# Kernel tuning notes

Hardware: AMD Instinct MI355X
Metric: run time of the kernel (lower is better)

The kernel has to match this reference:

```python
import jax, jax.numpy as jnp
import numpy as np

B, V, D, H = 128, 32, 64, 256
E = V * (V - 1)  # 992 directed edges (no self loops)
_edges = np.ones((V, V)) - np.eye(V)
SEND, RECV = np.where(_edges)  # each len E


def _mlp(x, w1, b1, w2, b2, w3, b3):
    h = jax.nn.relu(x @ w1.T + b1)
    h = jax.nn.relu(h @ w2.T + b2)
    return h @ w3.T + b3


def setup_inputs() -> dict:
    key = jax.random.key(0)
    ks = iter(jax.random.split(key, 48))
    def w(shape, scale=0.05):
        return jax.random.normal(next(ks), shape, jnp.float32) * scale
    d = {}
    d['inputs'] = jax.random.normal(next(ks), (B, V, D), jnp.float32)
    d['h0'] = jax.random.normal(next(ks), (B, E, H), jnp.float32) * 0.1
    d['c0'] = jax.random.normal(next(ks), (B, E, H), jnp.float32) * 0.1
    for name, ind in (('m1', D), ('m2', 2 * H), ('m3', H), ('m4', 3 * H)):
        d[name + 'w1'] = w((H, ind)); d[name + 'b1'] = jnp.full((H,), 0.1, jnp.float32)
        d[name + 'w2'] = w((H, H));   d[name + 'b2'] = jnp.full((H,), 0.1, jnp.float32)
        d[name + 'w3'] = w((H, H));   d[name + 'b3'] = jnp.full((H,), 0.1, jnp.float32)
    d['wih'] = w((4 * H, H)); d['whh'] = w((4 * H, H))
    d['bih'] = jnp.zeros((4 * H,), jnp.float32); d['bhh'] = jnp.zeros((4 * H,), jnp.float32)
    d['pw1'] = w((H, H)); d['pb1'] = jnp.full((H,), 0.1, jnp.float32)
    d['pw2'] = w((H, H)); d['pb2'] = jnp.full((H,), 0.1, jnp.float32)
    d['pw3'] = w((2, H)); d['pb3'] = jnp.full((2,), 0.1, jnp.float32)
    return d


def reference(inputs, h0, c0,
              m1w1, m1b1, m1w2, m1b2, m1w3, m1b3,
              m2w1, m2b1, m2w2, m2b2, m2w3, m2b3,
              m3w1, m3b1, m3w2, m3b2, m3w3, m3b3,
              m4w1, m4b1, m4w2, m4b2, m4w3, m4b3,
              wih, whh, bih, bhh,
              pw1, pb1, pw2, pb2, pw3, pb3):
    send, recv = jnp.asarray(SEND), jnp.asarray(RECV)
    # edge2node one-hot matrix [V, E] (fixed, non-trainable in original)
    e2n = (recv[None, :] == jnp.arange(V)[:, None]).astype(inputs.dtype)

    x = _mlp(inputs, m1w1, m1b1, m1w2, m1b2, m1w3, m1b3)          # [B,V,H]
    x = jnp.concatenate([x[:, send], x[:, recv]], axis=-1)         # [B,E,2H]
    x = _mlp(x, m2w1, m2b1, m2w2, m2b2, m2w3, m2b3)                # [B,E,H]
    x_skip = x
    x = jnp.einsum('ve,beh->bvh', e2n, x) / (V - 1)                # [B,V,H]
    x = _mlp(x, m3w1, m3b1, m3w2, m3b2, m3w3, m3b3)                # [B,V,H]
    x = jnp.concatenate([x[:, send], x[:, recv], x_skip], axis=-1)  # [B,E,3H]
    x = _mlp(x, m4w1, m4b1, m4w2, m4b2, m4w3, m4b3)                # [B,E,H]

    # single-step LSTM over B*E independent sequences of length 1
    gates = x @ wih.T + bih + h0 @ whh.T + bhh                     # [B,E,4H]
    i, f, g, o = jnp.split(gates, 4, axis=-1)
    c1 = jax.nn.sigmoid(f) * c0 + jax.nn.sigmoid(i) * jnp.tanh(g)
    h1 = jax.nn.sigmoid(o) * jnp.tanh(c1)

    prior_result = _mlp(h1, pw1, pb1, pw2, pb2, pw3, pb3)          # [B,E,2]
    return prior_result, h1, c1
```

## Files before the change

### kernel.cpp

```cpp
#include <hip/hip_runtime.h>
#include <math.h>

#define B_ 128
#define V_ 32
#define D_ 64
#define H_ 256
#define E_ 992
#define ME (B_*E_)
#define MV (B_*V_)

typedef __attribute__((ext_vector_type(8))) short bf8v;
typedef __attribute__((ext_vector_type(4))) float f4v;
typedef __attribute__((ext_vector_type(8))) unsigned short u16x8;

__device__ __forceinline__ unsigned short f2bf(float f) {
    union { float f; unsigned int u; } v; v.f = f;
    unsigned int u = v.u + 0x7FFFu + ((v.u >> 16) & 1u);
    return (unsigned short)(u >> 16);
}
__device__ __forceinline__ float bf2f(unsigned short h) {
    union { unsigned int u; float f; } v; v.u = ((unsigned int)h) << 16;
    return v.f;
}
__device__ __forceinline__ float sigf(float x) {
    x = fminf(fmaxf(x, -30.f), 30.f);
    return 1.f / (1.f + __expf(-x));
}
__device__ __forceinline__ float tanhf_fast(float x) {
    x = fminf(fmaxf(x, -15.f), 15.f);
    float e = __expf(2.f * x);
    return (e - 1.f) / (e + 1.f);
}
__device__ __forceinline__ void gl_lds16(const unsigned short* g, unsigned short* l) {
    __builtin_amdgcn_global_load_lds(
        (const __attribute__((address_space(1))) unsigned int*)g,
        (__attribute__((address_space(3))) unsigned int*)l, 16, 0, 0);
}

__device__ __forceinline__ int tidx(int row, int k) {
    return row * 256 + (k ^ ((row & 7) << 3));
}

__global__ __launch_bounds__(256)
void f2b_k(const float* __restrict__ s, unsigned short* __restrict__ d, int n4)
{
    const int g = blockIdx.x * 256 + threadIdx.x;
    if (g >= n4) return;
    const float4 v = ((const float4*)s)[g];
    ushort4 o;
    o.x = f2bf(v.x); o.y = f2bf(v.y); o.z = f2bf(v.z); o.w = f2bf(v.w);
    ((ushort4*)d)[g] = o;
}

__global__ __launch_bounds__(256)
void f2bs_k(const float* __restrict__ s, unsigned short* __restrict__ d,
            int rows, int cols4, int ld, int off)
{
    const int g = blockIdx.x * 256 + threadIdx.x;
    if (g >= rows * cols4) return;
    const int r = g / cols4, c4 = g - r * cols4;
    const float4 v = *(const float4*)(s + (size_t)r * ld + off + c4 * 4);
    ushort4 o;
    o.x = f2bf(v.x); o.y = f2bf(v.y); o.z = f2bf(v.z); o.w = f2bf(v.w);
    *(ushort4*)(d + (size_t)r * cols4 * 4 + c4 * 4) = o;
}

__global__ __launch_bounds__(256)
void gemm_k(const float* __restrict__ A, int lda,
            const float* __restrict__ W, int ldw,
            const float* __restrict__ bias,
            float* __restrict__ out,
            int M, int N, int K, int do_relu)
{
    __shared__ float As[32][68];
    __shared__ float Ws[32][68];
    const int m0 = blockIdx.x * 64;
    const int n0 = blockIdx.y * 64;
    const int t  = threadIdx.x;
    const int tx = t & 15, ty = t >> 4;
    const int lm = t >> 3;
    const int lk = (t & 7) * 4;

    float acc[4][4] = {};

    for (int k0 = 0; k0 < K; k0 += 32) {
        #pragma unroll
        for (int h = 0; h < 2; ++h) {
            const int m = m0 + lm + h * 32;
            const float4 v = *(const float4*)(A + (size_t)m * lda + k0 + lk);
            As[lk + 0][lm + h * 32] = v.x;
            As[lk + 1][lm + h * 32] = v.y;
            As[lk + 2][lm + h * 32] = v.z;
            As[lk + 3][lm + h * 32] = v.w;
            const int n = n0 + lm + h * 32;
            const float4 w = *(const float4*)(W + (size_t)n * ldw + k0 + lk);
            Ws[lk + 0][lm + h * 32] = w.x;
            Ws[lk + 1][lm + h * 32] = w.y;
            Ws[lk + 2][lm + h * 32] = w.z;
            Ws[lk + 3][lm + h * 32] = w.w;
        }
        __syncthreads();
        #pragma unroll
        for (int kk = 0; kk < 32; ++kk) {
            float a[4], b[4];
            #pragma unroll
            for (int i = 0; i < 4; ++i) a[i] = As[kk][ty * 4 + i];
            #pragma unroll
            for (int j = 0; j < 4; ++j) b[j] = Ws[kk][tx * 4 + j];
            #pragma unroll
            for (int i = 0; i < 4; ++i)
                #pragma unroll
                for (int j = 0; j < 4; ++j)
                    acc[i][j] = fmaf(a[i], b[j], acc[i][j]);
        }
        __syncthreads();
    }

    #pragma unroll
    for (int i = 0; i < 4; ++i) {
        const int m = m0 + ty * 4 + i;
        const size_t ob = (size_t)m * N;
        #pragma unroll
        for (int j = 0; j < 4; ++j) {
            const int n = n0 + tx * 4 + j;
            float v = acc[i][j];
            if (bias) v += bias[n];
            if (do_relu) v = fmaxf(v, 0.f);
            out[ob + n] = v;
        }
    }
}

template<int RELU, int EPI>
__device__ __forceinline__ void chain_gemm(
    unsigned short* T, unsigned short* Wst,
    const unsigned short* __restrict__ W, const float* __restrict__ bias,
    int m0, const float* __restrict__ ES, const float* __restrict__ ER)
{
    const int t = threadIdx.x, lane = t & 63, wid = t >> 6;
    const int r = wid >> 2, c = wid & 3;
    const int kof = (lane >> 4) * 8;
    const int ra = r * 64 + (lane & 15);
    const int q1 = t & 255, kp1 = t >> 8;

    f4v acc[4][4];
    #pragma unroll
    for (int i = 0; i < 4; ++i)
        #pragma unroll
        for (int j = 0; j < 4; ++j)
            acc[i][j] = (f4v){0.f, 0.f, 0.f, 0.f};

    gl_lds16(W + (size_t)q1 * 256 + kp1 * 8,       Wst + t * 8);
    gl_lds16(W + (size_t)q1 * 256 + (kp1 + 2) * 8, Wst + 4096 + t * 8);
    __syncthreads();
    int cur = 0;
    #pragma unroll
    for (int s = 0; s < 8; ++s) {
        if (s < 7) {
            const int k0 = (s + 1) * 32;
            gl_lds16(W + (size_t)q1 * 256 + k0 + kp1 * 8,       Wst + (cur ^ 1) * 8192 + t * 8);
            gl_lds16(W + (size_t)q1 * 256 + k0 + (kp1 + 2) * 8, Wst + (cur ^ 1) * 8192 + 4096 + t * 8);
        }
        bf8v a[4], b[4];
        #pragma unroll
        for (int f = 0; f < 4; ++f) {
            const int rr = ra + f * 16;
            a[f] = *(const bf8v*)&T[tidx(rr, s * 32 + kof)];
            b[f] = *(const bf8v*)&Wst[cur * 8192 + (lane >> 4) * 2048 + (c * 64 + f * 16 + (lane & 15)) * 8];
        }
        #pragma unroll
        for (int i = 0; i < 4; ++i)
            #pragma unroll
            for (int j = 0; j < 4; ++j)
                acc[i][j] = __builtin_amdgcn_mfma_f32_16x16x32_bf16(a[i], b[j], acc[i][j], 0, 0, 0);
        __syncthreads();
        cur ^= 1;
    }

    float bv[4];
    #pragma unroll
    for (int nf = 0; nf < 4; ++nf) bv[nf] = bias[c * 64 + nf * 16 + (lane & 15)];

    #pragma unroll
    for (int mf = 0; mf < 4; ++mf) {
        #pragma unroll
        for (int reg = 0; reg < 4; ++reg) {
            const int row = r * 64 + mf * 16 + (lane >> 4) * 4 + reg;
            size_t bs = 0, br = 0;
            if (EPI) {
                const int m  = m0 + row;
                const int bb = m / E_;
                const int e  = m - bb * E_;
                const int sS = e / 31;
                const int jj = e - sS * 31;
                const int rr = jj + (jj >= sS ? 1 : 0);
                bs = ((size_t)bb * V_ + sS) * H_;
                br = ((size_t)bb * V_ + rr) * H_;
            }
            #pragma unroll
            for (int nf = 0; nf < 4; ++nf) {
                const int n = c * 64 + nf * 16 + (lane & 15);
                float v = acc[mf][nf][reg] + bv[nf];
                if (EPI) v += ES[bs + n] + ER[br + n];
                if (RELU) v = fmaxf(v, 0.f);
                T[tidx(row, n)] = f2bf(v);
            }
        }
    }
    __syncthreads();
}

__global__ __launch_bounds__(512, 2)
void chain1_k(const float* __restrict__ Ys, const float* __restrict__ Yr,
              const float* __restrict__ b1,
              const unsigned short* __restrict__ w2, const float* __restrict__ b2,
              const unsigned short* __restrict__ w3, const float* __restrict__ b3,
              unsigned short* __restrict__ X2out)
{
    __shared__ alignas(16) unsigned short T[32768];
    __shared__ alignas(16) unsigned short Wst[16384];
    const int t  = threadIdx.x;
    const int m0 = blockIdx.x * 128;

    #pragma unroll
    for (int it = 0; it < 16; ++it) {
        const int q   = it * 512 + t;
        const int row = q >> 6;
        const int n4  = (q & 63) * 4;
        const int m  = m0 + row;
        const int bb = m / E_;
        const int e  = m - bb * E_;
        const int s  = e / 31;
        const int jj = e - s * 31;
        const int rv = jj + (jj >= s ? 1 : 0);
        const float4 ys = *(const float4*)&Ys[((size_t)bb * V_ + s)  * H_ + n4];
        const float4 yr = *(const float4*)&Yr[((size_t)bb * V_ + rv) * H_ + n4];
        const float4 bx = *(const float4*)&b1[n4];
        ushort4 o;
        o.x = f2bf(fmaxf(ys.x + yr.x + bx.x, 0.f));
        o.y = f2bf(fmaxf(ys.y + yr.y + bx.y, 0.f));
        o.z = f2bf(fmaxf(ys.z + yr.z + bx.z, 0.f));
        o.w = f2bf(fmaxf(ys.w + yr.w + bx.w, 0.f));
        *(ushort4*)&T[tidx(row, n4)] = o;
    }
    __syncthreads();

    chain_gemm<1, 0>(T, Wst, w2, b2, m0, nullptr, nullptr);
    chain_gemm<0, 0>(T, Wst, w3, b3, m0, nullptr, nullptr);

    #pragma unroll
    for (int it = 0; it < 8; ++it) {
        const int g   = it * 512 + t;
        const int row = g >> 5;
        const int kp  = (g & 31) * 8;
        *(u16x8*)&X2out[(size_t)(m0 + row) * 256 + kp] = *(const u16x8*)&T[tidx(row, kp)];
    }
}

__device__ __forceinline__ void lstm_pass(
    const unsigned short* T, unsigned short* Wst, unsigned short* Ast,
    const unsigned short* __restrict__ h0b,
    const unsigned short* __restrict__ wih, const unsigned short* __restrict__ whh,
    const float* __restrict__ bih, const float* __restrict__ bhh,
    const float* __restrict__ c0,
    float* __restrict__ h1, float* __restrict__ c1, unsigned short* __restrict__ h1b,
    int m0, int jc)
{
    const int t = threadIdx.x, lane = t & 63, wid = t >> 6;
    const int r = wid >> 2, c = wid & 3;
    const int kof = (lane >> 4) * 8;
    const int ra = r * 64 + (lane & 15);
    const int q1 = t & 255, kp1 = t >> 8;
    const size_t grow = (size_t)((q1 >> 6) * 256 + jc * 64 + (q1 & 63)) * 256;
    const int qa = t & 127, kpa = t >> 7;

    f4v acc[4][4];
    #pragma unroll
    for (int i = 0; i < 4; ++i)
        #pragma unroll
        for (int j = 0; j < 4; ++j)
            acc[i][j] = (f4v){0.f, 0.f, 0.f, 0.f};

    gl_lds16(wih + grow + kp1 * 8,       Wst + t * 8);
    gl_lds16(wih + grow + (kp1 + 2) * 8, Wst + 4096 + t * 8);
    __syncthreads();
    int cur = 0;
    #pragma unroll
    for (int s = 0; s < 16; ++s) {
        if (s < 15) {
            const int s2 = s + 1;
            const unsigned short* Wm = (s2 < 8) ? wih : whh;
            const int k0 = (s2 & 7) * 32;
            gl_lds16(Wm + grow + k0 + kp1 * 8,       Wst + (cur ^ 1) * 8192 + t * 8);
            gl_lds16(Wm + grow + k0 + (kp1 + 2) * 8, Wst + (cur ^ 1) * 8192 + 4096 + t * 8);
            if (s2 >= 8) {
                const int ka = (s2 - 8) * 32;
                gl_lds16(h0b + (size_t)(m0 + qa) * 256 + ka + kpa * 8, Ast + (cur ^ 1) * 4096 + t * 8);
            }
        }
        bf8v a[4], b[4];
        #pragma unroll
        for (int f = 0; f < 4; ++f) {
            const int rr = ra + f * 16;
            if (s < 8) a[f] = *(const bf8v*)&T[tidx(rr, s * 32 + kof)];
            else       a[f] = *(const bf8v*)&Ast[cur * 4096 + (lane >> 4) * 1024 + rr * 8];
            b[f] = *(const bf8v*)&Wst[cur * 8192 + (lane >> 4) * 2048 + (f * 64 + c * 16 + (lane & 15)) * 8];
        }
        #pragma unroll
        for (int i = 0; i < 4; ++i)
            #pragma unroll
            for (int g = 0; g < 4; ++g)
                acc[i][g] = __builtin_amdgcn_mfma_f32_16x16x32_bf16(a[i], b[g], acc[i][g], 0, 0, 0);
        __syncthreads();
        cur ^= 1;
    }

    const int j = jc * 64 + c * 16 + (lane & 15);
    const float bi0 = bih[j]       + bhh[j];
    const float bi1 = bih[256 + j] + bhh[256 + j];
    const float bi2 = bih[512 + j] + bhh[512 + j];
    const float bi3 = bih[768 + j] + bhh[768 + j];
    #pragma unroll
    for (int mf = 0; mf < 4; ++mf) {
        #pragma unroll
        for (int reg = 0; reg < 4; ++reg) {
            const int row = r * 64 + mf * 16 + (lane >> 4) * 4 + reg;
            const size_t o = (size_t)(m0 + row) * 256 + j;
            const float gi = acc[mf][0][reg] + bi0;
            const float gf = acc[mf][1][reg] + bi1;
            const float gg = acc[mf][2][reg] + bi2;
            const float go = acc[mf][3][reg] + bi3;
            const float cn = sigf(gf) * c0[o] + sigf(gi) * tanhf_fast(gg);
            const float hn = sigf(go) * tanhf_fast(cn);
            c1[o] = cn;
            h1[o] = hn;
            h1b[o] = f2bf(hn);
        }
    }
    __syncthreads();
}

__global__ __launch_bounds__(512, 2)
void chain2_k(const unsigned short* __restrict__ X2,
              const unsigned short* __restrict__ w41, const float* __restrict__ b41,
              const unsigned short* __restrict__ w42, const float* __restrict__ b42,
              const unsigned short* __restrict__ w43, const float* __restrict__ b43,
              const float* __restrict__ ZS, const float* __restrict__ ZR,
              const unsigned short* __restrict__ h0b,
              const unsigned short* __restrict__ wih, const unsigned short* __restrict__ whh,
              const float* __restrict__ bih, const float* __restrict__ bhh,
              const float* __restrict__ c0,
              float* __restrict__ h1, float* __restrict__ c1,
              unsigned short* __restrict__ h1b)
{
    __shared__ alignas(16) unsigned short T[32768];
    __shared__ alignas(16) unsigned short Wst[16384];
    __shared__ alignas(16) unsigned short Ast[8192];
    const int t  = threadIdx.x;
    const int m0 = blockIdx.x * 128;

    #pragma unroll
    for (int it = 0; it < 8; ++it) {
        const int g   = it * 512 + t;
        const int row = g >> 5;
        const int kp  = (g & 31) * 8;
        *(u16x8*)&T[tidx(row, kp)] = *(const u16x8*)&X2[(size_t)(m0 + row) * 256 + kp];
    }
    __syncthreads();

    chain_gemm<1, 1>(T, Wst, w41, b41, m0, ZS, ZR);
    chain_gemm<1, 0>(T, Wst, w42, b42, m0, nullptr, nullptr);
    chain_gemm<0, 0>(T, Wst, w43, b43, m0, nullptr, nullptr);

    for (int jc = 0; jc < 4; ++jc)
        lstm_pass(T, Wst, Ast, h0b, wih, whh, bih, bhh, c0, h1, c1, h1b, m0, jc);
}

__global__ __launch_bounds__(512, 2)
void prior_k(const unsigned short* __restrict__ Hin,
             const unsigned short* __restrict__ w1, const float* __restrict__ b1,
             const unsigned short* __restrict__ w2, const float* __restrict__ b2,
             const float* __restrict__ w3, const float* __restrict__ b3,
             float* __restrict__ out)
{
    __shared__ alignas(16) unsigned short T[32768];
    __shared__ alignas(16) unsigned short Wst[16384];
    const int t  = threadIdx.x;
    const int m0 = blockIdx.x * 128;

    #pragma unroll
    for (int it = 0; it < 8; ++it) {
        const int g   = it * 512 + t;
        const int row = g >> 5;
        const int kp  = (g & 31) * 8;
        *(u16x8*)&T[tidx(row, kp)] = *(const u16x8*)&Hin[(size_t)(m0 + row) * 256 + kp];
    }
    __syncthreads();

    chain_gemm<1, 0>(T, Wst, w1, b1, m0, nullptr, nullptr);
    chain_gemm<1, 0>(T, Wst, w2, b2, m0, nullptr, nullptr);

    const int row = t >> 2;
    const int kb  = (t & 3) * 64;
    float p0 = 0.f, p1 = 0.f;
    #pragma unroll
    for (int g = 0; g < 8; ++g) {
        const int k = kb + g * 8;
        const u16x8 v = *(const u16x8*)&T[tidx(row, k)];
        #pragma unroll
        for (int i = 0; i < 8; ++i) {
            const float x = bf2f(v[i]);
            p0 += x * w3[k + i];
            p1 += x * w3[256 + k + i];
        }
    }
    p0 += __shfl_xor(p0, 1); p0 += __shfl_xor(p0, 2);
    p1 += __shfl_xor(p1, 1); p1 += __shfl_xor(p1, 2);
    if ((t & 3) == 0) {
        out[(size_t)(m0 + row) * 2 + 0] = p0 + b3[0];
        out[(size_t)(m0 + row) * 2 + 1] = p1 + b3[1];
    }
}

__global__ __launch_bounds__(256)
void agg_k(const unsigned short* __restrict__ X2, float* __restrict__ outv)
{
    const int g = blockIdx.x * 256 + threadIdx.x;
    const int h = g & 255;
    const int v = (g >> 8) & 31;
    const int b = g >> 13;
    float s = 0.f;
    #pragma unroll
    for (int snd = 0; snd < 32; ++snd) {
        if (snd == v) continue;
        const int e = snd * 31 + v - (snd < v ? 1 : 0);
        s += bf2f(X2[((size_t)b * E_ + e) * H_ + h]);
    }
    outv[g] = s * (1.f / 31.f);
}

extern "C" void kernel_launch(void* const* d_in, const int* in_sizes, int n_in,
                              void* d_out, int out_size, void* d_ws, size_t ws_size,
                              hipStream_t stream)
{
    const float* inputs = (const float*)d_in[0];
    const float* h0     = (const float*)d_in[1];
    const float* c0     = (const float*)d_in[2];
    const float* m1w1 = (const float*)d_in[3];  const float* m1b1 = (const float*)d_in[4];
    const float* m1w2 = (const float*)d_in[5];  const float* m1b2 = (const float*)d_in[6];
    const float* m1w3 = (const float*)d_in[7];  const float* m1b3 = (const float*)d_in[8];
    const float* m2w1 = (const float*)d_in[9];  const float* m2b1 = (const float*)d_in[10];
    const float* m2w2 = (const float*)d_in[11]; const float* m2b2 = (const float*)d_in[12];
    const float* m2w3 = (const float*)d_in[13]; const float* m2b3 = (const float*)d_in[14];
    const float* m3w1 = (const float*)d_in[15]; const float* m3b1 = (const float*)d_in[16];
    const float* m3w2 = (const float*)d_in[17]; const float* m3b2 = (const float*)d_in[18];
    const float* m3w3 = (const float*)d_in[19]; const float* m3b3 = (const float*)d_in[20];
    const float* m4w1 = (const float*)d_in[21]; const float* m4b1 = (const float*)d_in[22];
    const float* m4w2 = (const float*)d_in[23]; const float* m4b2 = (const float*)d_in[24];
    const float* m4w3 = (const float*)d_in[25]; const float* m4b3 = (const float*)d_in[26];
    const float* wih  = (const float*)d_in[27]; const float* whh  = (const float*)d_in[28];
    const float* bih  = (const float*)d_in[29]; const float* bhh  = (const float*)d_in[30];
    const float* pw1  = (const float*)d_in[31]; const float* pb1  = (const float*)d_in[32];
    const float* pw2  = (const float*)d_in[33]; const float* pb2  = (const float*)d_in[34];
    const float* pw3  = (const float*)d_in[35]; const float* pb3  = (const float*)d_in[36];

    float* out   = (float*)d_out;
    float* prior = out;
    float* h1    = out + (size_t)ME * 2;
    float* c1    = h1 + (size_t)ME * H_;

    float* S0 = (float*)d_ws;
    float* S1 = S0 + (size_t)MV * H_;
    float* S2 = S1 + (size_t)MV * H_;
    float* S3 = S2 + (size_t)MV * H_;
    unsigned short* EA = (unsigned short*)(S3 + (size_t)MV * H_);
    unsigned short* EB = EA + (size_t)ME * H_;
    unsigned short* EC = EB + (size_t)ME * H_;
    unsigned short* cw22 = EC + (size_t)ME * H_;
    unsigned short* cw23 = cw22 + 65536;
    unsigned short* cw41 = cw23 + 65536;
    unsigned short* cw42 = cw41 + 65536;
    unsigned short* cw43 = cw42 + 65536;
    unsigned short* cpw1 = cw43 + 65536;
    unsigned short* cpw2 = cpw1 + 65536;
    unsigned short* cwih = cpw2 + 65536;
    unsigned short* cwhh = cwih + 262144;

    const dim3 blk(256);
    const dim3 blk5(512);
    const dim3 gV(MV / 64, 4);
    const dim3 gC(ME / 128);

    f2b_k<<<64, blk, 0, stream>>>(m2w2, cw22, 16384);
    f2b_k<<<64, blk, 0, stream>>>(m2w3, cw23, 16384);
    f2bs_k<<<64, blk, 0, stream>>>(m4w1, cw41, 256, 64, 768, 512);
    f2b_k<<<64, blk, 0, stream>>>(m4w2, cw42, 16384);
    f2b_k<<<64, blk, 0, stream>>>(m4w3, cw43, 16384);
    f2b_k<<<64, blk, 0, stream>>>(pw1, cpw1, 16384);
    f2b_k<<<64, blk, 0, stream>>>(pw2, cpw2, 16384);
    f2b_k<<<256, blk, 0, stream>>>(wih, cwih, 65536);
    f2b_k<<<256, blk, 0, stream>>>(whh, cwhh, 65536);
    f2b_k<<<ME * H_ / 1024, blk, 0, stream>>>(h0, EB, ME * H_ / 4);

    gemm_k<<<gV, blk, 0, stream>>>(inputs, 64, m1w1, 64, m1b1, S0, MV, 256, 64, 1);
    gemm_k<<<gV, blk, 0, stream>>>(S0, 256, m1w2, 256, m1b2, S1, MV, 256, 256, 1);
    gemm_k<<<gV, blk, 0, stream>>>(S1, 256, m1w3, 256, m1b3, S0, MV, 256, 256, 0);

    gemm_k<<<gV, blk, 0, stream>>>(S0, 256, m2w1,       512, nullptr, S2, MV, 256, 256, 0);
    gemm_k<<<gV, blk, 0, stream>>>(S0, 256, m2w1 + 256, 512, nullptr, S3, MV, 256, 256, 0);

    chain1_k<<<gC, blk5, 0, stream>>>(S2, S3, m2b1, cw22, m2b2, cw23, m2b3, EA);

    agg_k<<<MV * H_ / 256, blk, 0, stream>>>(EA, S0);
    gemm_k<<<gV, blk, 0, stream>>>(S0, 256, m3w1, 256, m3b1, S1, MV, 256, 256, 1);
    gemm_k<<<gV, blk, 0, stream>>>(S1, 256, m3w2, 256, m3b2, S0, MV, 256, 256, 1);
    gemm_k<<<gV, blk, 0, stream>>>(S0, 256, m3w3, 256, m3b3, S1, MV, 256, 256, 0);

    gemm_k<<<gV, blk, 0, stream>>>(S1, 256, m4w1,       768, nullptr, S2, MV, 256, 256, 0);
    gemm_k<<<gV, blk, 0, stream>>>(S1, 256, m4w1 + 256, 768, nullptr, S3, MV, 256, 256, 0);

    chain2_k<<<gC, blk5, 0, stream>>>(EA, cw41, m4b1, cw42, m4b2, cw43, m4b3,
                                      S2, S3, EB, cwih, cwhh, bih, bhh, c0, h1, c1, EC);

    prior_k<<<gC, blk5, 0, stream>>>(EC, cpw1, pb1, cpw2, pb2, pw3, pb3, prior);
}
```

Before: 1.382 ms.

## Load MFMA weight fragments directly from global into registers, halve chain tiles

The fused chain kernels (edge MLPs, LSTM, prior MLP) no longer stage weights through LDS with global_load_lds double buffering. Each wave now reads its B fragments straight from global memory (L2-resident bf16 weights) into registers, prefetching one k-step ahead, and the LSTM h0 operand is read the same way. The row tile drops from 128 to 64 with 256-thread blocks, which cuts LDS use and removes the per-k-step barriers, so more blocks can be resident per CU. The nine weight conversion launches are merged into two batched kernels. In exchange, weight fetches are repeated per wave from global/L2 instead of shared through LDS, and global-load latency now sits closer to the MFMA loop.

Result: slower. 3.935 ms (+184.8%).

```diff
diff --git a/kernel.cpp b/kernel.cpp
--- a/kernel.cpp
+++ b/kernel.cpp
@@ -31,14 +31,43 @@
     float e = __expf(2.f * x);
     return (e - 1.f) / (e + 1.f);
 }
-__device__ __forceinline__ void gl_lds16(const unsigned short* g, unsigned short* l) {
-    __builtin_amdgcn_global_load_lds(
-        (const __attribute__((address_space(1))) unsigned int*)g,
-        (__attribute__((address_space(3))) unsigned int*)l, 16, 0, 0);
-}
 
 __device__ __forceinline__ int tidx(int row, int k) {
     return row * 256 + (k ^ ((row & 7) << 3));
+}
+
+__global__ __launch_bounds__(256)
+void convW7_k(const float* __restrict__ s0, const float* __restrict__ s1,
+              const float* __restrict__ s2, const float* __restrict__ s3,
+              const float* __restrict__ s4, const float* __restrict__ s5,
+              const float* __restrict__ s6, unsigned short* __restrict__ d)
+{
+    const int y = blockIdx.y;
+    const int g = blockIdx.x * 256 + threadIdx.x;
+    float4 v;
+    if (y == 2) {
+        const int r = g >> 6, c4 = (g & 63) * 4;
+        v = *(const float4*)(s2 + (size_t)r * 768 + 512 + c4);
+    } else {
+        const float* s = (y == 0) ? s0 : (y == 1) ? s1 : (y == 3) ? s3 :
+                         (y == 4) ? s4 : (y == 5) ? s5 : s6;
+        v = ((const float4*)s)[g];
+    }
+    ushort4 o;
+    o.x = f2bf(v.x); o.y = f2bf(v.y); o.z = f2bf(v.z); o.w = f2bf(v.w);
+    ((ushort4*)(d + (size_t)y * 65536))[g] = o;
+}
+
+__global__ __launch_bounds__(256)
+void convIH_k(const float* __restrict__ wih, const float* __restrict__ whh,
+              unsigned short* __restrict__ d)
+{
+    const int y = blockIdx.y;
+    const int g = blockIdx.x * 256 + threadIdx.x;
+    const float4 v = ((const float4*)(y ? whh : wih))[g];
+    ushort4 o;
+    o.x = f2bf(v.x); o.y = f2bf(v.y); o.z = f2bf(v.z); o.w = f2bf(v.w);
+    ((ushort4*)(d + (size_t)y * 262144))[g] = o;
 }
 
 __global__ __launch_bounds__(256)
@@ -50,19 +79,6 @@
     ushort4 o;
     o.x = f2bf(v.x); o.y = f2bf(v.y); o.z = f2bf(v.z); o.w = f2bf(v.w);
     ((ushort4*)d)[g] = o;
-}
-
-__global__ __launch_bounds__(256)
-void f2bs_k(const float* __restrict__ s, unsigned short* __restrict__ d,
-            int rows, int cols4, int ld, int off)
-{
-    const int g = blockIdx.x * 256 + threadIdx.x;
-    if (g >= rows * cols4) return;
-    const int r = g / cols4, c4 = g - r * cols4;
-    const float4 v = *(const float4*)(s + (size_t)r * ld + off + c4 * 4);
-    ushort4 o;
-    o.x = f2bf(v.x); o.y = f2bf(v.y); o.z = f2bf(v.z); o.w = f2bf(v.w);
-    *(ushort4*)(d + (size_t)r * cols4 * 4 + c4 * 4) = o;
 }
 
 __global__ __launch_bounds__(256)
@@ -132,16 +148,14 @@
 }
 
 template<int RELU, int EPI>
-__device__ __forceinline__ void chain_gemm(
-    unsigned short* T, unsigned short* Wst,
+__device__ __forceinline__ void chain_layer(
+    unsigned short* T,
     const unsigned short* __restrict__ W, const float* __restrict__ bias,
     int m0, const float* __restrict__ ES, const float* __restrict__ ER)
 {
-    const int t = threadIdx.x, lane = t & 63, wid = t >> 6;
-    const int r = wid >> 2, c = wid & 3;
-    const int kof = (lane >> 4) * 8;
-    const int ra = r * 64 + (lane & 15);
-    const int q1 = t & 255, kp1 = t >> 8;
+    const int t = threadIdx.x, lane = t & 63, c = t >> 6;
+    const int laneN = lane & 15, kof = (lane >> 4) * 8;
+    const unsigned short* wb = W + (size_t)(c * 64 + laneN) * 256 + kof;
 
     f4v acc[4][4];
     #pragma unroll
@@ -150,42 +164,40 @@
         for (int j = 0; j < 4; ++j)
             acc[i][j] = (f4v){0.f, 0.f, 0.f, 0.f};
 
-    gl_lds16(W + (size_t)q1 * 256 + kp1 * 8,       Wst + t * 8);
-    gl_lds16(W + (size_t)q1 * 256 + (kp1 + 2) * 8, Wst + 4096 + t * 8);
+    bf8v bc[4];
+    #pragma unroll
+    for (int f = 0; f < 4; ++f) bc[f] = *(const bf8v*)(wb + f * 4096);
+
+    #pragma unroll
+    for (int s = 0; s < 8; ++s) {
+        bf8v bn[4];
+        if (s < 7) {
+            #pragma unroll
+            for (int f = 0; f < 4; ++f) bn[f] = *(const bf8v*)(wb + f * 4096 + (s + 1) * 32);
+        }
+        bf8v a[4];
+        #pragma unroll
+        for (int i = 0; i < 4; ++i) a[i] = *(const bf8v*)&T[tidx(i * 16 + laneN, s * 32 + kof)];
+        #pragma unroll
+        for (int i = 0; i < 4; ++i)
+            #pragma unroll
+            for (int j = 0; j < 4; ++j)
+                acc[i][j] = __builtin_amdgcn_mfma_f32_16x16x32_bf16(a[i], bc[j], acc[i][j], 0, 0, 0);
+        #pragma unroll
+        for (int f = 0; f < 4; ++f) bc[f] = bn[f];
+    }
+
     __syncthreads();
-    int cur = 0;
-    #pragma unroll
-    for (int s = 0; s < 8; ++s) {
-        if (s < 7) {
-            const int k0 = (s + 1) * 32;
-            gl_lds16(W + (size_t)q1 * 256 + k0 + kp1 * 8,       Wst + (cur ^ 1) * 8192 + t * 8);
-            gl_lds16(W + (size_t)q1 * 256 + k0 + (kp1 + 2) * 8, Wst + (cur ^ 1) * 8192 + 4096 + t * 8);
-        }
-        bf8v a[4], b[4];
-        #pragma unroll
-        for (int f = 0; f < 4; ++f) {
-            const int rr = ra + f * 16;
-            a[f] = *(const bf8v*)&T[tidx(rr, s * 32 + kof)];
-            b[f] = *(const bf8v*)&Wst[cur * 8192 + (lane >> 4) * 2048 + (c * 64 + f * 16 + (lane & 15)) * 8];
-        }
-        #pragma unroll
-        for (int i = 0; i < 4; ++i)
-            #pragma unroll
-            for (int j = 0; j < 4; ++j)
-                acc[i][j] = __builtin_amdgcn_mfma_f32_16x16x32_bf16(a[i], b[j], acc[i][j], 0, 0, 0);
-        __syncthreads();
-        cur ^= 1;
-    }
 
     float bv[4];
     #pragma unroll
-    for (int nf = 0; nf < 4; ++nf) bv[nf] = bias[c * 64 + nf * 16 + (lane & 15)];
-
-    #pragma unroll
-    for (int mf = 0; mf < 4; ++mf) {
+    for (int j = 0; j < 4; ++j) bv[j] = bias[c * 64 + j * 16 + laneN];
+
+    #pragma unroll
+    for (int i = 0; i < 4; ++i) {
         #pragma unroll
         for (int reg = 0; reg < 4; ++reg) {
-            const int row = r * 64 + mf * 16 + (lane >> 4) * 4 + reg;
+            const int row = i * 16 + (lane >> 4) * 4 + reg;
             size_t bs = 0, br = 0;
             if (EPI) {
                 const int m  = m0 + row;
@@ -198,9 +210,9 @@
                 br = ((size_t)bb * V_ + rr) * H_;
             }
             #pragma unroll
-            for (int nf = 0; nf < 4; ++nf) {
-                const int n = c * 64 + nf * 16 + (lane & 15);
-                float v = acc[mf][nf][reg] + bv[nf];
+            for (int j = 0; j < 4; ++j) {
+                const int n = c * 64 + j * 16 + laneN;
+                float v = acc[i][j][reg] + bv[j];
                 if (EPI) v += ES[bs + n] + ER[br + n];
                 if (RELU) v = fmaxf(v, 0.f);
                 T[tidx(row, n)] = f2bf(v);
@@ -210,21 +222,95 @@
     __syncthreads();
 }
 
-__global__ __launch_bounds__(512, 2)
+__device__ __forceinline__ void lstm_pass(
+    const unsigned short* T,
+    const unsigned short* __restrict__ h0b,
+    const unsigned short* __restrict__ wih, const unsigned short* __restrict__ whh,
+    const float* __restrict__ bih, const float* __restrict__ bhh,
+    const float* __restrict__ c0,
+    float* __restrict__ h1, float* __restrict__ c1, unsigned short* __restrict__ h1b,
+    int m0, int jc)
+{
+    const int t = threadIdx.x, lane = t & 63, c = t >> 6;
+    const int laneN = lane & 15, kof = (lane >> 4) * 8;
+    const unsigned short* wbi = wih + (size_t)(jc * 64 + c * 16 + laneN) * 256 + kof;
+    const unsigned short* wbh = whh + (size_t)(jc * 64 + c * 16 + laneN) * 256 + kof;
+    const unsigned short* ab  = h0b + (size_t)(m0 + laneN) * 256 + kof;
+
+    f4v acc[4][4];
+    #pragma unroll
+    for (int i = 0; i < 4; ++i)
+        #pragma unroll
+        for (int g = 0; g < 4; ++g)
+            acc[i][g] = (f4v){0.f, 0.f, 0.f, 0.f};
+
+    bf8v bc[4];
+    #pragma unroll
+    for (int g = 0; g < 4; ++g) bc[g] = *(const bf8v*)(wbi + (size_t)g * 65536);
+
+    #pragma unroll
+    for (int s = 0; s < 16; ++s) {
+        bf8v bn[4];
+        if (s < 15) {
+            const int s2 = s + 1;
+            #pragma unroll
+            for (int g = 0; g < 4; ++g)
+                bn[g] = (s2 < 8) ? *(const bf8v*)(wbi + (size_t)g * 65536 + s2 * 32)
+                                 : *(const bf8v*)(wbh + (size_t)g * 65536 + (s2 - 8) * 32);
+        }
+        bf8v a[4];
+        #pragma unroll
+        for (int i = 0; i < 4; ++i) {
+            if (s < 8) a[i] = *(const bf8v*)&T[tidx(i * 16 + laneN, s * 32 + kof)];
+            else       a[i] = *(const bf8v*)(ab + (size_t)i * 4096 + (s - 8) * 32);
+        }
+        #pragma unroll
+        for (int i = 0; i < 4; ++i)
+            #pragma unroll
+            for (int g = 0; g < 4; ++g)
+                acc[i][g] = __builtin_amdgcn_mfma_f32_16x16x32_bf16(a[i], bc[g], acc[i][g], 0, 0, 0);
+        #pragma unroll
+        for (int g = 0; g < 4; ++g) bc[g] = bn[g];
+    }
+
+    const int j = jc * 64 + c * 16 + laneN;
+    const float bi0 = bih[j]       + bhh[j];
+    const float bi1 = bih[256 + j] + bhh[256 + j];
+    const float bi2 = bih[512 + j] + bhh[512 + j];
+    const float bi3 = bih[768 + j] + bhh[768 + j];
+    #pragma unroll
+    for (int i = 0; i < 4; ++i) {
+        #pragma unroll
+        for (int reg = 0; reg < 4; ++reg) {
+            const int row = i * 16 + (lane >> 4) * 4 + reg;
+            const size_t o = (size_t)(m0 + row) * 256 + j;
+            const float gi = acc[i][0][reg] + bi0;
+            const float gf = acc[i][1][reg] + bi1;
+            const float gg = acc[i][2][reg] + bi2;
+            const float go = acc[i][3][reg] + bi3;
+            const float cn = sigf(gf) * c0[o] + sigf(gi) * tanhf_fast(gg);
+            const float hn = sigf(go) * tanhf_fast(cn);
+            c1[o] = cn;
+            h1[o] = hn;
+            h1b[o] = f2bf(hn);
+        }
+    }
+}
+
+__global__ __launch_bounds__(256, 3)
 void chain1_k(const float* __restrict__ Ys, const float* __restrict__ Yr,
               const float* __restrict__ b1,
               const unsigned short* __restrict__ w2, const float* __restrict__ b2,
               const unsigned short* __restrict__ w3, const float* __restrict__ b3,
               unsigned short* __restrict__ X2out)
 {
-    __shared__ alignas(16) unsigned short T[32768];
-    __shared__ alignas(16) unsigned short Wst[16384];
+    __shared__ alignas(16) unsigned short T[16384];
     const int t  = threadIdx.x;
-    const int m0 = blockIdx.x * 128;
+    const int m0 = blockIdx.x * 64;
 
     #pragma unroll
     for (int it = 0; it < 16; ++it) {
-        const int q   = it * 512 + t;
+        const int q   = it * 256 + t;
         const int row = q >> 6;
         const int n4  = (q & 63) * 4;
         const int m  = m0 + row;
@@ -245,102 +331,19 @@
     }
     __syncthreads();
 
-    chain_gemm<1, 0>(T, Wst, w2, b2, m0, nullptr, nullptr);
-    chain_gemm<0, 0>(T, Wst, w3, b3, m0, nullptr, nullptr);
+    chain_layer<1, 0>(T, w2, b2, m0, nullptr, nullptr);
+    chain_layer<0, 0>(T, w3, b3, m0, nullptr, nullptr);
 
     #pragma unroll
     for (int it = 0; it < 8; ++it) {
-        const int g   = it * 512 + t;
+        const int g   = it * 256 + t;
         const int row = g >> 5;
         const int kp  = (g & 31) * 8;
         *(u16x8*)&X2out[(size_t)(m0 + row) * 256 + kp] = *(const u16x8*)&T[tidx(row, kp)];
     }
 }
 
-__device__ __forceinline__ void lstm_pass(
-    const unsigned short* T, unsigned short* Wst, unsigned short* Ast,
-    const unsigned short* __restrict__ h0b,
-    const unsigned short* __restrict__ wih, const unsigned short* __restrict__ whh,
-    const float* __restrict__ bih, const float* __restrict__ bhh,
-    const float* __restrict__ c0,
-    float* __restrict__ h1, float* __restrict__ c1, unsigned short* __restrict__ h1b,
-    int m0, int jc)
-{
-    const int t = threadIdx.x, lane = t & 63, wid = t >> 6;
-    const int r = wid >> 2, c = wid & 3;
-    const int kof = (lane >> 4) * 8;
-    const int ra = r * 64 + (lane & 15);
-    const int q1 = t & 255, kp1 = t >> 8;
-    const size_t grow = (size_t)((q1 >> 6) * 256 + jc * 64 + (q1 & 63)) * 256;
-    const int qa = t & 127, kpa = t >> 7;
-
-    f4v acc[4][4];
-    #pragma unroll
-    for (int i = 0; i < 4; ++i)
-        #pragma unroll
-        for (int j = 0; j < 4; ++j)
-            acc[i][j] = (f4v){0.f, 0.f, 0.f, 0.f};
-
-    gl_lds16(wih + grow + kp1 * 8,       Wst + t * 8);
-    gl_lds16(wih + grow + (kp1 + 2) * 8, Wst + 4096 + t * 8);
-    __syncthreads();
-    int cur = 0;
-    #pragma unroll
-    for (int s = 0; s < 16; ++s) {
-        if (s < 15) {
-            const int s2 = s + 1;
-            const unsigned short* Wm = (s2 < 8) ? wih : whh;
-            const int k0 = (s2 & 7) * 32;
-            gl_lds16(Wm + grow + k0 + kp1 * 8,       Wst + (cur ^ 1) * 8192 + t * 8);
-            gl_lds16(Wm + grow + k0 + (kp1 + 2) * 8, Wst + (cur ^ 1) * 8192 + 4096 + t * 8);
-            if (s2 >= 8) {
-                const int ka = (s2 - 8) * 32;
-                gl_lds16(h0b + (size_t)(m0 + qa) * 256 + ka + kpa * 8, Ast + (cur ^ 1) * 4096 + t * 8);
-            }
-        }
-        bf8v a[4], b[4];
-        #pragma unroll
-        for (int f = 0; f < 4; ++f) {
-            const int rr = ra + f * 16;
-            if (s < 8) a[f] = *(const bf8v*)&T[tidx(rr, s * 32 + kof)];
-            else       a[f] = *(const bf8v*)&Ast[cur * 4096 + (lane >> 4) * 1024 + rr * 8];
-            b[f] = *(const bf8v*)&Wst[cur * 8192 + (lane >> 4) * 2048 + (f * 64 + c * 16 + (lane & 15)) * 8];
-        }
-        #pragma unroll
-        for (int i = 0; i < 4; ++i)
-            #pragma unroll
-            for (int g = 0; g < 4; ++g)
-                acc[i][g] = __builtin_amdgcn_mfma_f32_16x16x32_bf16(a[i], b[g], acc[i][g], 0, 0, 0);
-        __syncthreads();
-        cur ^= 1;
-    }
-
-    const int j = jc * 64 + c * 16 + (lane & 15);
-    const float bi0 = bih[j]       + bhh[j];
-    const float bi1 = bih[256 + j] + bhh[256 + j];
-    const float bi2 = bih[512 + j] + bhh[512 + j];
-    const float bi3 = bih[768 + j] + bhh[768 + j];
-    #pragma unroll
-    for (int mf = 0; mf < 4; ++mf) {
-        #pragma unroll
-        for (int reg = 0; reg < 4; ++reg) {
-            const int row = r * 64 + mf * 16 + (lane >> 4) * 4 + reg;
-            const size_t o = (size_t)(m0 + row) * 256 + j;
-            const float gi = acc[mf][0][reg] + bi0;
-            const float gf = acc[mf][1][reg] + bi1;
-            const float gg = acc[mf][2][reg] + bi2;
-            const float go = acc[mf][3][reg] + bi3;
-            const float cn = sigf(gf) * c0[o] + sigf(gi) * tanhf_fast(gg);
-            const float hn = sigf(go) * tanhf_fast(cn);
-            c1[o] = cn;
-            h1[o] = hn;
-            h1b[o] = f2bf(hn);
-        }
-    }
-    __syncthreads();
-}
-
-__global__ __launch_bounds__(512, 2)
+__global__ __launch_bounds__(256, 3)
 void chain2_k(const unsigned short* __restrict__ X2,
               const unsigned short* __restrict__ w41, const float* __restrict__ b41,
               const unsigned short* __restrict__ w42, const float* __restrict__ b42,
@@ -353,52 +356,50 @@
               float* __restrict__ h1, float* __restrict__ c1,
               unsigned short* __restrict__ h1b)
 {
-    __shared__ alignas(16) unsigned short T[32768];
-    __shared__ alignas(16) unsigned short Wst[16384];
-    __shared__ alignas(16) unsigned short Ast[8192];
+    __shared__ alignas(16) unsigned short T[16384];
     const int t  = threadIdx.x;
-    const int m0 = blockIdx.x * 128;
+    const int m0 = blockIdx.x * 64;
 
     #pragma unroll
     for (int it = 0; it < 8; ++it) {
-        const int g   = it * 512 + t;
+        const int g   = it * 256 + t;
         const int row = g >> 5;
         const int kp  = (g & 31) * 8;
         *(u16x8*)&T[tidx(row, kp)] = *(const u16x8*)&X2[(size_t)(m0 + row) * 256 + kp];
     }
     __syncthreads();
 
-    chain_gemm<1, 1>(T, Wst, w41, b41, m0, ZS, ZR);
-    chain_gemm<1, 0>(T, Wst, w42, b42, m0, nullptr, nullptr);
-    chain_gemm<0, 0>(T, Wst, w43, b43, m0, nullptr, nullptr);
-
+    chain_layer<1, 1>(T, w41, b41, m0, ZS, ZR);
+    chain_layer<1, 0>(T, w42, b42, m0, nullptr, nullptr);
+    chain_layer<0, 0>(T, w43, b43, m0, nullptr, nullptr);
+
+    #pragma unroll
     for (int jc = 0; jc < 4; ++jc)
-        lstm_pass(T, Wst, Ast, h0b, wih, whh, bih, bhh, c0, h1, c1, h1b, m0, jc);
-}
-
-__global__ __launch_bounds__(512, 2)
+        lstm_pass(T, h0b, wih, whh, bih, bhh, c0, h1, c1, h1b, m0, jc);
+}
+
+__global__ __launch_bounds__(256, 3)
 void prior_k(const unsigned short* __restrict__ Hin,
              const unsigned short* __restrict__ w1, const float* __restrict__ b1,
              const unsigned short* __restrict__ w2, const float* __restrict__ b2,
              const float* __restrict__ w3, const float* __restrict__ b3,
              float* __restrict__ out)
 {
-    __shared__ alignas(16) unsigned short T[32768];
-    __shared__ alignas(16) unsigned short Wst[16384];
+    __shared__ alignas(16) unsigned short T[16384];
     const int t  = threadIdx.x;
-    const int m0 = blockIdx.x * 128;
+    const int m0 = blockIdx.x * 64;
 
     #pragma unroll
     for (int it = 0; it < 8; ++it) {
-        const int g   = it * 512 + t;
+        const int g   = it * 256 + t;
         const int row = g >> 5;
         const int kp  = (g & 31) * 8;
         *(u16x8*)&T[tidx(row, kp)] = *(const u16x8*)&Hin[(size_t)(m0 + row) * 256 + kp];
     }
     __syncthreads();
 
-    chain_gemm<1, 0>(T, Wst, w1, b1, m0, nullptr, nullptr);
-    chain_gemm<1, 0>(T, Wst, w2, b2, m0, nullptr, nullptr);
+    chain_layer<1, 0>(T, w1, b1, m0, nullptr, nullptr);
+    chain_layer<1, 0>(T, w2, b2, m0, nullptr, nullptr);
 
     const int row = t >> 2;
     const int kb  = (t & 3) * 64;
@@ -476,30 +477,24 @@
     unsigned short* EA = (unsigned short*)(S3 + (size_t)MV * H_);
     unsigned short* EB = EA + (size_t)ME * H_;
     unsigned short* EC = EB + (size_t)ME * H_;
-    unsigned short* cw22 = EC + (size_t)ME * H_;
-    unsigned short* cw23 = cw22 + 65536;
-    unsigned short* cw41 = cw23 + 65536;
-    unsigned short* cw42 = cw41 + 65536;
-    unsigned short* cw43 = cw42 + 65536;
-    unsigned short* cpw1 = cw43 + 65536;
-    unsigned short* cpw2 = cpw1 + 65536;
-    unsigned short* cwih = cpw2 + 65536;
-    unsigned short* cwhh = cwih + 262144;
+    unsigned short* CW = EC + (size_t)ME * H_;
+    unsigned short* cw22 = CW;
+    unsigned short* cw23 = CW + 1 * 65536;
+    unsigned short* cw41 = CW + 2 * 65536;
+    unsigned short* cw42 = CW + 3 * 65536;
+    unsigned short* cw43 = CW + 4 * 65536;
+    unsigned short* cpw1 = CW + 5 * 65536;
+    unsigned short* cpw2 = CW + 6 * 65536;
+    unsigned short* cIH  = CW + 7 * 65536;
+    unsigned short* cwih = cIH;
+    unsigned short* cwhh = cIH + 262144;
 
     const dim3 blk(256);
-    const dim3 blk5(512);
     const dim3 gV(MV / 64, 4);
-    const dim3 gC(ME / 128);
-
-    f2b_k<<<64, blk, 0, stream>>>(m2w2, cw22, 16384);
-    f2b_k<<<64, blk, 0, stream>>>(m2w3, cw23, 16384);
-    f2bs_k<<<64, blk, 0, stream>>>(m4w1, cw41, 256, 64, 768, 512);
-    f2b_k<<<64, blk, 0, stream>>>(m4w2, cw42, 16384);
-    f2b_k<<<64, blk, 0, stream>>>(m4w3, cw43, 16384);
-    f2b_k<<<64, blk, 0, stream>>>(pw1, cpw1, 16384);
-    f2b_k<<<64, blk, 0, stream>>>(pw2, cpw2, 16384);
-    f2b_k<<<256, blk, 0, stream>>>(wih, cwih, 65536);
-    f2b_k<<<256, blk, 0, stream>>>(whh, cwhh, 65536);
+    const dim3 gC(ME / 64);
+
+    convW7_k<<<dim3(64, 7), blk, 0, stream>>>(m2w2, m2w3, m4w1, m4w2, m4w3, pw1, pw2, CW);
+    convIH_k<<<dim3(256, 2), blk, 0, stream>>>(wih, whh, cIH);
     f2b_k<<<ME * H_ / 1024, blk, 0, stream>>>(h0, EB, ME * H_ / 4);
 
     gemm_k<<<gV, blk, 0, stream>>>(inputs, 64, m1w1, 64, m1b1, S0, MV, 256, 64, 1);
@@ -509,7 +504,7 @@
     gemm_k<<<gV, blk, 0, stream>>>(S0, 256, m2w1,       512, nullptr, S2, MV, 256, 256, 0);
     gemm_k<<<gV, blk, 0, stream>>>(S0, 256, m2w1 + 256, 512, nullptr, S3, MV, 256, 256, 0);
 
-    chain1_k<<<gC, blk5, 0, stream>>>(S2, S3, m2b1, cw22, m2b2, cw23, m2b3, EA);
+    chain1_k<<<gC, blk, 0, stream>>>(S2, S3, m2b1, cw22, m2b2, cw23, m2b3, EA);
 
     agg_k<<<MV * H_ / 256, blk, 0, stream>>>(EA, S0);
     gemm_k<<<gV, blk, 0, stream>>>(S0, 256, m3w1, 256, m3b1, S1, MV, 256, 256, 1);
@@ -519,8 +514,8 @@
     gemm_k<<<gV, blk, 0, stream>>>(S1, 256, m4w1,       768, nullptr, S2, MV, 256, 256, 0);
     gemm_k<<<gV, blk, 0, stream>>>(S1, 256, m4w1 + 256, 768, nullptr, S3, MV, 256, 256, 0);
 
-    chain2_k<<<gC, blk5, 0, stream>>>(EA, cw41, m4b1, cw42, m4b2, cw43, m4b3,
-                                      S2, S3, EB, cwih, cwhh, bih, bhh, c0, h1, c1, EC);
-
-    prior_k<<<gC, blk5, 0, stream>>>(EC, cpw1, pb1, cpw2, pb2, pw3, pb3, prior);
-}
+    chain2_k<<<gC, blk, 0, stream>>>(EA, cw41, m4b1, cw42, m4b2, cw43, m4b3,
+                                     S2, S3, EB, cwih, cwhh, bih, bhh, c0, h1, c1, EC);
+
+    prior_k<<<gC, blk, 0, stream>>>(EC, cpw1, pb1, cpw2, pb2, pw3, pb3, prior);
+}
```
